# Optimization experiments

Hardware: AMD Instinct MI355X
Metric: run time of the kernel (lower is better)

Reference implementation:

```python
import jax, jax.numpy as jnp
import numpy as np

SCALE = 1.0 / np.sqrt(1024.0).astype(np.float32)


def setup_inputs() -> dict:
    key = jax.random.key(0)
    k1, k2, k3, k4, k5, k6 = jax.random.split(key, 6)
    B, Lq, Lk, D_in, D = 8, 2048, 2048, 1024, 256
    data1 = jax.random.normal(k1, (B, Lq, D_in), dtype=jnp.float32)
    data2 = jax.random.normal(k2, (B, Lk, D), dtype=jnp.float32)
    Wq = jax.random.normal(k3, (D_in, D), dtype=jnp.float32) * (1.0 / np.sqrt(D_in))
    bq = jax.random.normal(k4, (D,), dtype=jnp.float32) * 0.01
    Wk = jax.random.normal(k5, (D, D), dtype=jnp.float32) * (1.0 / np.sqrt(D))
    bk = jax.random.normal(k6, (D,), dtype=jnp.float32) * 0.01
    return {"data1": data1, "data2": data2, "Wq": Wq, "bq": bq, "Wk": Wk, "bk": bk}


def reference(data1, data2, Wq, bq, Wk, bk):
    # query: [B, Lq, D], key: [B, Lk, D]
    query = jnp.einsum('bli,id->bld', data1, Wq) + bq
    key = jnp.einsum('bli,id->bld', data2, Wk) + bk
    # scores: [B, Lq, Lk], scaled by sqrt(1024) as in the original
    scores = jnp.einsum('bqd,bkd->bqk', query, key) * SCALE
    attn = jax.nn.softmax(scores, axis=-1)
    # key reused as value; fused residual add with query
    context = jnp.einsum('bqk,bkd->bqd', attn, key) + query
    return context
```

## Files before the change

kernel.cpp:

```cpp
#include <hip/hip_runtime.h>
#include <hip/hip_bf16.h>

typedef __bf16 bf16x8 __attribute__((ext_vector_type(8)));
typedef __bf16 bf16x2 __attribute__((ext_vector_type(2)));
typedef unsigned short u16x8 __attribute__((ext_vector_type(8)));
typedef unsigned short u16x4 __attribute__((ext_vector_type(4)));
typedef float f32x4 __attribute__((ext_vector_type(4)));
typedef float f32x16 __attribute__((ext_vector_type(16)));

#define MFMA(a, b, c) __builtin_amdgcn_mfma_f32_16x16x32_bf16(a, b, c, 0, 0, 0)
#define MFMA32(a, b, c) __builtin_amdgcn_mfma_f32_32x32x16_bf16(a, b, c, 0, 0, 0)

#define LQ 2048
#define DD 256

static __device__ __forceinline__ float bf2f(unsigned short u) {
  union { unsigned int i; float f; } x; x.i = ((unsigned int)u) << 16; return x.f;
}
static __device__ __forceinline__ unsigned short f2bf(float f) {
  union { float f; unsigned int i; } x; x.f = f;
  unsigned int r = x.i + 0x7fffu + ((x.i >> 16) & 1u);
  return (unsigned short)(r >> 16);
}
static __device__ __forceinline__ void gll16(const void* g, void* l) {
  __builtin_amdgcn_global_load_lds(
      (const __attribute__((address_space(1))) unsigned int*)g,
      (__attribute__((address_space(3))) unsigned int*)l, 16, 0, 0);
}
static __device__ __forceinline__ unsigned pack2(float a, float b) {
  union { bf16x2 v; unsigned u; } x;
  x.v[0] = (__bf16)a; x.v[1] = (__bf16)b;
  return x.u;
}

__global__ void wt2_kernel(const float* __restrict__ Wq, unsigned short* __restrict__ WqT,
                           const float* __restrict__ Wk, unsigned short* __restrict__ WkT) {
  int id = blockIdx.x * 256 + threadIdx.x;
  if (id < 262144) {
    int n = id >> 10, k = id & 1023;
    WqT[id] = f2bf(Wq[k * 256 + n]);
  } else {
    int j = id - 262144;
    int n = j >> 8, k = j & 255;
    WkT[j] = f2bf(Wk[k * 256 + n]);
  }
}

__global__ __launch_bounds__(256) void proj_kernel(
    const float* __restrict__ A, const unsigned short* __restrict__ WT,
    const float* __restrict__ bias, unsigned short* __restrict__ outb,
    unsigned short* __restrict__ outT, int Kd) {
  __shared__ unsigned short A_s[2][64 * 32];
  __shared__ unsigned short B_s[2][128 * 32];
  const int tid = threadIdx.x;
  const int w = tid >> 6, lane = tid & 63, g = lane >> 4, c = lane & 15;
  const int m0 = (blockIdx.x >> 1) * 64, n0 = (blockIdx.x & 1) * 128;
  const int wr = (w >> 1) * 32, wc = (w & 1) * 64;

  f32x4 acc[2][4];
  const f32x4 z4 = {0.f, 0.f, 0.f, 0.f};
#pragma unroll
  for (int i = 0; i < 2; i++)
#pragma unroll
    for (int j = 0; j < 4; j++) acc[i][j] = z4;

  const int row_a = tid >> 2, k0a = (tid & 3) * 8;
  const unsigned swz_a = (unsigned)((row_a & 7) << 4);
  const float* asrc = A + (long)(m0 + row_a) * Kd + k0a;
  const int brow0 = w * 32 + (lane >> 2);

#define GLLB(buf, ks_)                                                         \
  _Pragma("unroll") for (int j = 0; j < 2; j++) {                              \
    const int brow = brow0 + j * 16;                                           \
    gll16((const char*)WT + (long)(n0 + brow) * (long)(Kd * 2) + (ks_) * 64 +  \
              (((lane & 3) * 16) ^ ((brow & 3) << 4)),                         \
          (char*)B_s[buf] + w * 2048 + j * 1024);                              \
  }

#define WRA(buf, plo, phi)                                                     \
  {                                                                            \
    bf16x8 t;                                                                  \
    _Pragma("unroll") for (int jj = 0; jj < 4; jj++) {                         \
      t[jj] = (__bf16)(plo)[jj]; t[4 + jj] = (__bf16)(phi)[jj];                \
    }                                                                          \
    *(bf16x8*)((char*)A_s[buf] +                                               \
               (((unsigned)(row_a * 64 + k0a * 2)) ^ swz_a)) = t;              \
  }

#define COMPUTE(buf)                                                           \
  {                                                                            \
    bf16x8 af[2], bfr[4];                                                      \
    _Pragma("unroll") for (int rf = 0; rf < 2; rf++) {                         \
      const int row = wr + rf * 16 + c;                                        \
      af[rf] = *(const bf16x8*)((char*)A_s[buf] +                              \
               (((unsigned)(row * 64 + g * 16)) ^ ((row & 7) << 4)));          \
    }                                                                          \
    _Pragma("unroll") for (int cf = 0; cf < 4; cf++) {                         \
      const int row = wc + cf * 16 + c;                                        \
      bfr[cf] = *(const bf16x8*)((char*)B_s[buf] + row * 64 +                  \
               (((unsigned)(g * 16)) ^ ((unsigned)((row & 3) << 4))));         \
    }                                                                          \
    _Pragma("unroll") for (int rf = 0; rf < 2; rf++)                           \
      _Pragma("unroll") for (int cf = 0; cf < 4; cf++)                         \
        acc[rf][cf] = MFMA(af[rf], bfr[cf], acc[rf][cf]);                      \
  }

  const int nk = Kd >> 5;
  f32x4 pe0, pe1, po0, po1;
  pe0 = *(const f32x4*)(asrc);       pe1 = *(const f32x4*)(asrc + 4);
  GLLB(0, 0);
  po0 = *(const f32x4*)(asrc + 32);  po1 = *(const f32x4*)(asrc + 36);
  WRA(0, pe0, pe1);
  pe0 = *(const f32x4*)(asrc + 64);  pe1 = *(const f32x4*)(asrc + 68);
  __syncthreads();

  for (int t = 0; t < nk; t += 2) {
    GLLB(1, t + 1);
    WRA(1, po0, po1);
    if (t + 3 < nk) {
      po0 = *(const f32x4*)(asrc + (t + 3) * 32);
      po1 = *(const f32x4*)(asrc + (t + 3) * 32 + 4);
    }
    COMPUTE(0);
    __syncthreads();
    if (t + 2 < nk) {
      GLLB(0, t + 2);
      WRA(0, pe0, pe1);
      if (t + 4 < nk) {
        pe0 = *(const f32x4*)(asrc + (t + 4) * 32);
        pe1 = *(const f32x4*)(asrc + (t + 4) * 32 + 4);
      }
    }
    COMPUTE(1);
    __syncthreads();
  }
#undef GLLB
#undef WRA
#undef COMPUTE

#pragma unroll
  for (int cf = 0; cf < 4; cf++) {
    const int col = n0 + wc + cf * 16 + c;
    const float bv = bias[col];
#pragma unroll
    for (int rf = 0; rf < 2; rf++) {
      const int row0 = m0 + wr + rf * 16 + g * 4;
      unsigned short pk[4];
#pragma unroll
      for (int i = 0; i < 4; i++) {
        float v = acc[rf][cf][i] + bv;
        pk[i] = f2bf(v);
        outb[(long)(row0 + i) * 256 + col] = pk[i];
      }
      if (outT) {
        const int b = row0 >> 11;
        const int key0 = row0 & 2047;
        unsigned long long packed = (unsigned long long)pk[0] |
                                    ((unsigned long long)pk[1] << 16) |
                                    ((unsigned long long)pk[2] << 32) |
                                    ((unsigned long long)pk[3] << 48);
        *(unsigned long long*)(outT + ((long)(b * 256 + col) * LQ + key0)) = packed;
      }
    }
  }
}

template <int NSPLIT>
__global__ __launch_bounds__(256, 2) void attn_kernel(
    const unsigned short* __restrict__ Qb, const unsigned short* __restrict__ Kb,
    const unsigned short* __restrict__ KTb, unsigned short* __restrict__ Op,
    float* __restrict__ out, float* __restrict__ ML) {
  constexpr int KS = 2048 / NSPLIT;
  constexpr int NT = KS / 32;
  constexpr int NBLK = 128 * NSPLIT;
  __shared__ char Ks[2][16384];
  __shared__ char KTs[2][16384];
  const int tid = threadIdx.x;
  const int w = tid >> 6, lane = tid & 63;
  const int l5 = lane >> 5, q31 = lane & 31;
  const int lid = (blockIdx.x & 7) * (NBLK / 8) + (blockIdx.x >> 3);
  const int ksplit = lid & (NSPLIT - 1), qg = lid / NSPLIT;
  const int b = qg >> 4;
  const long qrow0 = (long)qg * 128;
  const int kbase = ksplit * KS;
  const float CS = 0.03125f * 1.4426950408889634f;
  const float THRM = 8.0f / CS;

  bf16x8 qf[16];
  {
    const unsigned short* qp = Qb + (qrow0 + w * 32 + q31) * DD + l5 * 8;
#pragma unroll
    for (int s = 0; s < 16; s++) qf[s] = *(const bf16x8*)(qp + s * 16);
  }
  f32x16 o[8];
#pragma unroll
  for (int t = 0; t < 8; t++) o[t] = (f32x16)(0.f);
  float m_ = -1e30f, l_ = 0.f;

  const char* kb_b = (const char*)(Kb + (long)b * LQ * DD);
  const char* kt_b = (const char*)(KTb + (long)b * DD * LQ);

#define STAGE(buf, kt_)                                                          \
  {                                                                              \
    const int k0_ = kbase + (kt_) * 32;                                          \
    const char* kbp_ = kb_b + (long)(k0_ + q31) * 512 + l5 * 16;                 \
    _Pragma("unroll") for (int i = 0; i < 4; i++) {                              \
      const int sl = w * 4 + i;                                                  \
      gll16(kbp_ + sl * 32, Ks[buf] + sl * 1024);                                \
    }                                                                            \
    _Pragma("unroll") for (int i = 0; i < 4; i++) {                              \
      const int th = w * 4 + i;                                                  \
      gll16(kt_b + (long)((th >> 1) * 32 + q31) * 4096 + (long)k0_ * 2 +         \
                (th & 1) * 32 + l5 * 16,                                         \
            KTs[buf] + th * 1024);                                               \
    }                                                                            \
  }

  STAGE(0, 0);
  for (int kt = 0; kt < NT; kt++) {
    const int cur = kt & 1;
    __syncthreads();
    if (kt + 1 < NT) STAGE(cur ^ 1, kt + 1);

    const char* kr = Ks[cur] + lane * 16;
    f32x16 s = (f32x16)(0.f);
#pragma unroll
    for (int sl = 0; sl < 16; sl++) {
      bf16x8 kf = *(const bf16x8*)(kr + sl * 1024);
      s = MFMA32(kf, qf[sl], s);
    }

    float mx = s[0];
#pragma unroll
    for (int r = 1; r < 16; r++) mx = fmaxf(mx, s[r]);
    mx = fmaxf(mx, __shfl_xor(mx, 32));
    if (__any(mx > m_ + THRM)) {
      float mn = fmaxf(m_, mx);
      float al = exp2f((m_ - mn) * CS);
      m_ = mn;
      l_ *= al;
#pragma unroll
      for (int t = 0; t < 8; t++) o[t] *= al;
    }
    const float mCS = m_ * CS;
    float p[16];
    float ls = 0.f;
#pragma unroll
    for (int r = 0; r < 16; r++) {
      p[r] = exp2f(s[r] * CS - mCS);
      ls += p[r];
    }
    l_ += ls;

    unsigned pk[8];
#pragma unroll
    for (int j = 0; j < 8; j++) pk[j] = pack2(p[2 * j], p[2 * j + 1]);
    unsigned x0 = (unsigned)__shfl_xor((int)pk[0], 32);
    unsigned x1 = (unsigned)__shfl_xor((int)pk[1], 32);
    unsigned x2 = (unsigned)__shfl_xor((int)pk[2], 32);
    unsigned x3 = (unsigned)__shfl_xor((int)pk[3], 32);
    unsigned x4 = (unsigned)__shfl_xor((int)pk[4], 32);
    unsigned x5 = (unsigned)__shfl_xor((int)pk[5], 32);
    unsigned x6 = (unsigned)__shfl_xor((int)pk[6], 32);
    unsigned x7 = (unsigned)__shfl_xor((int)pk[7], 32);
    union { unsigned u[4]; bf16x8 v; } pf0, pf1;
    const bool hi = (l5 != 0);
    pf0.u[0] = hi ? x2 : pk[0];
    pf0.u[1] = hi ? x3 : pk[1];
    pf0.u[2] = hi ? pk[2] : x0;
    pf0.u[3] = hi ? pk[3] : x1;
    pf1.u[0] = hi ? x6 : pk[4];
    pf1.u[1] = hi ? x7 : pk[5];
    pf1.u[2] = hi ? pk[6] : x4;
    pf1.u[3] = hi ? pk[7] : x5;

    const char* vr = KTs[cur] + lane * 16;
#pragma unroll
    for (int t = 0; t < 8; t++) {
      bf16x8 v0 = *(const bf16x8*)(vr + (t * 2) * 1024);
      bf16x8 v1 = *(const bf16x8*)(vr + (t * 2 + 1) * 1024);
      o[t] = MFMA32(v0, pf0.v, o[t]);
      o[t] = MFMA32(v1, pf1.v, o[t]);
    }
  }
#undef STAGE

  l_ += __shfl_xor(l_, 32);

  const long orow = (qrow0 + w * 32 + q31) * (long)DD;
  if (ksplit == NSPLIT - 1) {
    float* op = out + orow;
#pragma unroll
    for (int t = 0; t < 8; t++)
#pragma unroll
      for (int r = 0; r < 16; r++)
        op[t * 32 + (r & 3) + 8 * (r >> 2) + 4 * l5] = o[t][r];
  } else {
    unsigned short* opb = Op + (long)ksplit * (16384 * 256) + orow;
#pragma unroll
    for (int t = 0; t < 8; t++)
#pragma unroll
      for (int r = 0; r < 16; r++)
        opb[t * 32 + (r & 3) + 8 * (r >> 2) + 4 * l5] = f2bf(o[t][r]);
  }
  if (lane < 32) {
    float* mlp = ML + (long)(qg * NSPLIT + ksplit) * 256;
    mlp[w * 32 + q31] = m_;
    mlp[128 + w * 32 + q31] = l_;
  }
}

template <int NSPLIT>
__global__ __launch_bounds__(256) void merge_kernel(
    const unsigned short* __restrict__ Op, const float* __restrict__ ML,
    const unsigned short* __restrict__ Qb, float* __restrict__ out) {
  const float CS = 0.03125f * 1.4426950408889634f;
  const long gid = (long)blockIdx.x * 256 + threadIdx.x;
  const long idx = gid * 8;
  const int row = (int)(idx >> 8);
  const int qg = row >> 7, qr = row & 127;
  const float* mlb = ML + (long)(qg * NSPLIT) * 256;
  float mv[NSPLIT], lv[NSPLIT];
#pragma unroll
  for (int k = 0; k < NSPLIT; k++) {
    mv[k] = mlb[k * 256 + qr];
    lv[k] = mlb[k * 256 + 128 + qr];
  }
  float M = mv[0];
#pragma unroll
  for (int k = 1; k < NSPLIT; k++) M = fmaxf(M, mv[k]);
  float ek[NSPLIT], wsum = 0.f;
#pragma unroll
  for (int k = 0; k < NSPLIT; k++) {
    ek[k] = exp2f((mv[k] - M) * CS);
    wsum += ek[k] * lv[k];
  }
  const float inv = 1.0f / wsum;
  float acc[8];
  {
    f32x4 pa = *(const f32x4*)(out + idx);
    f32x4 pb = *(const f32x4*)(out + idx + 4);
#pragma unroll
    for (int e = 0; e < 4; e++) {
      acc[e] = ek[NSPLIT - 1] * pa[e];
      acc[4 + e] = ek[NSPLIT - 1] * pb[e];
    }
  }
#pragma unroll
  for (int k = 0; k < NSPLIT - 1; k++) {
    u16x8 p = *(const u16x8*)(Op + (long)k * (16384 * 256) + idx);
#pragma unroll
    for (int e = 0; e < 8; e++) acc[e] += ek[k] * bf2f(p[e]);
  }
  u16x8 qv = *(const u16x8*)(Qb + idx);
  f32x4 ra, rb;
#pragma unroll
  for (int e = 0; e < 4; e++) ra[e] = acc[e] * inv + bf2f(qv[e]);
#pragma unroll
  for (int e = 0; e < 4; e++) rb[e] = acc[4 + e] * inv + bf2f(qv[4 + e]);
  *(f32x4*)(out + idx) = ra;
  *(f32x4*)(out + idx + 4) = rb;
}

extern "C" void kernel_launch(void* const* d_in, const int* in_sizes, int n_in,
                              void* d_out, int out_size, void* d_ws, size_t ws_size,
                              hipStream_t stream) {
  (void)in_sizes; (void)n_in; (void)out_size;
  const float* data1 = (const float*)d_in[0];
  const float* data2 = (const float*)d_in[1];
  const float* Wq = (const float*)d_in[2];
  const float* bq = (const float*)d_in[3];
  const float* Wk = (const float*)d_in[4];
  const float* bk = (const float*)d_in[5];
  float* out = (float*)d_out;

  char* ws = (char*)d_ws;
  unsigned short* Qb  = (unsigned short*)(ws);
  unsigned short* Kb  = (unsigned short*)(ws + (8ull << 20));
  unsigned short* KTb = (unsigned short*)(ws + (16ull << 20));
  unsigned short* WqT = (unsigned short*)(ws + (24ull << 20));
  unsigned short* WkT = (unsigned short*)(ws + (24ull << 20) + (512u << 10));
  unsigned short* Op  = (unsigned short*)(ws + (25ull << 20));

  wt2_kernel<<<dim3(1280), dim3(256), 0, stream>>>(Wq, WqT, Wk, WkT);
  proj_kernel<<<dim3(512), dim3(256), 0, stream>>>(data1, WqT, bq, Qb,
                                                   (unsigned short*)nullptr, 1024);
  proj_kernel<<<dim3(512), dim3(256), 0, stream>>>(data2, WkT, bk, Kb, KTb, 256);

  if (ws_size >= (50ull << 20)) {
    float* MLb = (float*)(ws + (49ull << 20));
    attn_kernel<4><<<dim3(512), dim3(256), 0, stream>>>(Qb, Kb, KTb, Op, out, MLb);
    merge_kernel<4><<<dim3(2048), dim3(256), 0, stream>>>(Op, MLb, Qb, out);
  } else {
    float* MLb = (float*)(ws + (33ull << 20));
    attn_kernel<2><<<dim3(256), dim3(256), 0, stream>>>(Qb, Kb, KTb, Op, out, MLb);
    merge_kernel<2><<<dim3(2048), dim3(256), 0, stream>>>(Op, MLb, Qb, out);
  }
}
```

Measured before the change: 110.4 us.

## Split QK MFMA chain, tree-reduce softmax max/sum, store all split partials as bf16

Splits the QK^T MFMA accumulation into two independent chains to shorten the dependency latency. Replaces the serial max and sum reductions with tree reductions. When the workspace is large enough, every K-split writes its partial output as bf16 instead of the last split writing fp32 into out, so the merge kernel reads only bf16 partials. This cuts fp32 partial traffic but adds a bf16 rounding step and depends on the workspace size.

```diff
diff --git a/kernel.cpp b/kernel.cpp
--- a/kernel.cpp
+++ b/kernel.cpp
@@ -165,7 +165,7 @@
   }
 }
 
-template <int NSPLIT>
+template <int NSPLIT, bool ALLBF>
 __global__ __launch_bounds__(256, 2) void attn_kernel(
     const unsigned short* __restrict__ Qb, const unsigned short* __restrict__ Kb,
     const unsigned short* __restrict__ KTb, unsigned short* __restrict__ Op,
@@ -223,17 +223,24 @@
     if (kt + 1 < NT) STAGE(cur ^ 1, kt + 1);
 
     const char* kr = Ks[cur] + lane * 16;
-    f32x16 s = (f32x16)(0.f);
-#pragma unroll
-    for (int sl = 0; sl < 16; sl++) {
-      bf16x8 kf = *(const bf16x8*)(kr + sl * 1024);
-      s = MFMA32(kf, qf[sl], s);
-    }
-
-    float mx = s[0];
-#pragma unroll
-    for (int r = 1; r < 16; r++) mx = fmaxf(mx, s[r]);
-    mx = fmaxf(mx, __shfl_xor(mx, 32));
+    f32x16 sa = (f32x16)(0.f), sb = (f32x16)(0.f);
+#pragma unroll
+    for (int sl = 0; sl < 8; sl++) {
+      bf16x8 kfa = *(const bf16x8*)(kr + sl * 1024);
+      bf16x8 kfb = *(const bf16x8*)(kr + (sl + 8) * 1024);
+      sa = MFMA32(kfa, qf[sl], sa);
+      sb = MFMA32(kfb, qf[sl + 8], sb);
+    }
+    f32x16 s = sa + sb;
+
+    float m8[8];
+#pragma unroll
+    for (int r = 0; r < 8; r++) m8[r] = fmaxf(s[2 * r], s[2 * r + 1]);
+#pragma unroll
+    for (int st = 4; st >= 1; st >>= 1)
+#pragma unroll
+      for (int r = 0; r < st; r++) m8[r] = fmaxf(m8[r], m8[r + st]);
+    float mx = fmaxf(m8[0], __shfl_xor(m8[0], 32));
     if (__any(mx > m_ + THRM)) {
       float mn = fmaxf(m_, mx);
       float al = exp2f((m_ - mn) * CS);
@@ -244,13 +251,16 @@
     }
     const float mCS = m_ * CS;
     float p[16];
-    float ls = 0.f;
-#pragma unroll
-    for (int r = 0; r < 16; r++) {
-      p[r] = exp2f(s[r] * CS - mCS);
-      ls += p[r];
-    }
-    l_ += ls;
+#pragma unroll
+    for (int r = 0; r < 16; r++) p[r] = exp2f(s[r] * CS - mCS);
+    float a8[8];
+#pragma unroll
+    for (int r = 0; r < 8; r++) a8[r] = p[2 * r] + p[2 * r + 1];
+#pragma unroll
+    for (int st = 4; st >= 1; st >>= 1)
+#pragma unroll
+      for (int r = 0; r < st; r++) a8[r] += a8[r + st];
+    l_ += a8[0];
 
     unsigned pk[8];
 #pragma unroll
@@ -288,7 +298,7 @@
   l_ += __shfl_xor(l_, 32);
 
   const long orow = (qrow0 + w * 32 + q31) * (long)DD;
-  if (ksplit == NSPLIT - 1) {
+  if (!ALLBF && ksplit == NSPLIT - 1) {
     float* op = out + orow;
 #pragma unroll
     for (int t = 0; t < 8; t++)
@@ -310,7 +320,7 @@
   }
 }
 
-template <int NSPLIT>
+template <int NSPLIT, bool ALLBF>
 __global__ __launch_bounds__(256) void merge_kernel(
     const unsigned short* __restrict__ Op, const float* __restrict__ ML,
     const unsigned short* __restrict__ Qb, float* __restrict__ out) {
@@ -337,7 +347,16 @@
   }
   const float inv = 1.0f / wsum;
   float acc[8];
-  {
+  if (ALLBF) {
+#pragma unroll
+    for (int e = 0; e < 8; e++) acc[e] = 0.f;
+#pragma unroll
+    for (int k = 0; k < NSPLIT; k++) {
+      u16x8 p = *(const u16x8*)(Op + (long)k * (16384 * 256) + idx);
+#pragma unroll
+      for (int e = 0; e < 8; e++) acc[e] += ek[k] * bf2f(p[e]);
+    }
+  } else {
     f32x4 pa = *(const f32x4*)(out + idx);
     f32x4 pb = *(const f32x4*)(out + idx + 4);
 #pragma unroll
@@ -345,12 +364,12 @@
       acc[e] = ek[NSPLIT - 1] * pa[e];
       acc[4 + e] = ek[NSPLIT - 1] * pb[e];
     }
-  }
-#pragma unroll
-  for (int k = 0; k < NSPLIT - 1; k++) {
-    u16x8 p = *(const u16x8*)(Op + (long)k * (16384 * 256) + idx);
-#pragma unroll
-    for (int e = 0; e < 8; e++) acc[e] += ek[k] * bf2f(p[e]);
+#pragma unroll
+    for (int k = 0; k < NSPLIT - 1; k++) {
+      u16x8 p = *(const u16x8*)(Op + (long)k * (16384 * 256) + idx);
+#pragma unroll
+      for (int e = 0; e < 8; e++) acc[e] += ek[k] * bf2f(p[e]);
+    }
   }
   u16x8 qv = *(const u16x8*)(Qb + idx);
   f32x4 ra, rb;
@@ -387,13 +406,17 @@
                                                    (unsigned short*)nullptr, 1024);
   proj_kernel<<<dim3(512), dim3(256), 0, stream>>>(data2, WkT, bk, Kb, KTb, 256);
 
-  if (ws_size >= (50ull << 20)) {
+  if (ws_size >= (58ull << 20)) {
+    float* MLb = (float*)(ws + (57ull << 20));
+    attn_kernel<4, true><<<dim3(512), dim3(256), 0, stream>>>(Qb, Kb, KTb, Op, out, MLb);
+    merge_kernel<4, true><<<dim3(2048), dim3(256), 0, stream>>>(Op, MLb, Qb, out);
+  } else if (ws_size >= (50ull << 20)) {
     float* MLb = (float*)(ws + (49ull << 20));
-    attn_kernel<4><<<dim3(512), dim3(256), 0, stream>>>(Qb, Kb, KTb, Op, out, MLb);
-    merge_kernel<4><<<dim3(2048), dim3(256), 0, stream>>>(Op, MLb, Qb, out);
+    attn_kernel<4, false><<<dim3(512), dim3(256), 0, stream>>>(Qb, Kb, KTb, Op, out, MLb);
+    merge_kernel<4, false><<<dim3(2048), dim3(256), 0, stream>>>(Op, MLb, Qb, out);
   } else {
     float* MLb = (float*)(ws + (33ull << 20));
-    attn_kernel<2><<<dim3(256), dim3(256), 0, stream>>>(Qb, Kb, KTb, Op, out, MLb);
-    merge_kernel<2><<<dim3(2048), dim3(256), 0, stream>>>(Op, MLb, Qb, out);
-  }
-}
+    attn_kernel<2, false><<<dim3(256), dim3(256), 0, stream>>>(Qb, Kb, KTb, Op, out, MLb);
+    merge_kernel<2, false><<<dim3(2048), dim3(256), 0, stream>>>(Op, MLb, Qb, out);
+  }
+}
```

Result: slower. 123.8 us (+12.2%).
